# Optimization experiments

Hardware: AMD Instinct MI355X
Metric: run time of the kernel (lower is better)

## Reference

```python
import jax, jax.numpy as jnp
import numpy as np
from jax import lax

BN_EPS = 1e-5
ARC_EPS = 1e-7
M = 0.5   # margin
S = 64.0  # scale


def _conv_block(x, w, g, b, a, stride):
    # Conv2d(bias=False, VALID) + BatchNorm2d (training mode, batch stats) + PReLU
    y = lax.conv_general_dilated(x, w, (stride, stride), 'VALID',
                                 dimension_numbers=('NCHW', 'OIHW', 'NCHW'))
    mu = y.mean((0, 2, 3), keepdims=True)
    var = ((y - mu) ** 2).mean((0, 2, 3), keepdims=True)
    y = (y - mu) * lax.rsqrt(var + BN_EPS) * g.reshape(1, -1, 1, 1) + b.reshape(1, -1, 1, 1)
    return jnp.where(y > 0, y, a * y)


def setup_inputs() -> dict:
    key = jax.random.key(0)
    ks = jax.random.split(key, 16)
    N = 4096
    d = {}
    d['x'] = jax.random.normal(ks[0], (N, 1, 28, 28), jnp.float32)
    d['labels'] = jax.random.randint(ks[1], (N,), 0, 10)
    conv_shapes = [(32, 1, 1, 1), (64, 32, 3, 3), (32, 64, 1, 1),
                   (64, 32, 3, 3), (32, 64, 1, 1), (64, 32, 3, 3)]
    for i, s in enumerate(conv_shapes):
        fan_in = s[1] * s[2] * s[3]
        d[f'cw{i}'] = jax.random.normal(ks[2 + i], s, jnp.float32) / np.sqrt(fan_in)
        d[f'bg{i}'] = jnp.ones((s[0],), jnp.float32)
        d[f'bb{i}'] = jnp.zeros((s[0],), jnp.float32)
        d[f'pa{i}'] = jnp.full((), 0.25, jnp.float32)  # nn.PReLU() single param
    d['lw1'] = jax.random.normal(ks[8], (128, 1024), jnp.float32) * (1.0 / np.sqrt(1024))
    d['lg1'] = jnp.ones((128,), jnp.float32)
    d['lb1'] = jnp.zeros((128,), jnp.float32)
    d['pl1'] = jnp.full((), 0.25, jnp.float32)
    d['lw2'] = jax.random.normal(ks[9], (2, 128), jnp.float32) * (1.0 / np.sqrt(128))
    d['lb2'] = jnp.zeros((2,), jnp.float32)
    d['aw'] = jax.random.normal(ks[10], (10, 2), jnp.float32) * 0.2  # ArcLoss fc weight (out, in)
    return d


def reference(x, labels, cw0, cw1, cw2, cw3, cw4, cw5,
              bg0, bb0, bg1, bb1, bg2, bb2, bg3, bb3, bg4, bb4, bg5, bb5,
              pa0, pa1, pa2, pa3, pa4, pa5,
              lw1, lg1, lb1, pl1, lw2, lb2, aw):
    strides = (1, 2, 1, 2, 1, 1)
    ws = (cw0, cw1, cw2, cw3, cw4, cw5)
    gs = (bg0, bg1, bg2, bg3, bg4, bg5)
    bs = (bb0, bb1, bb2, bb3, bb4, bb5)
    pas = (pa0, pa1, pa2, pa3, pa4, pa5)
    h = x
    for w, g, b, a, st in zip(ws, gs, bs, pas, strides):
        h = _conv_block(h, w, g, b, a, st)  # final: (N, 64, 4, 4)
    flat = h.reshape(h.shape[0], -1)        # (N, 1024)
    z = flat @ lw1.T                         # (N, 128)
    mu = z.mean(0)
    var = ((z - mu) ** 2).mean(0)
    z = (z - mu) * lax.rsqrt(var + BN_EPS) * lg1 + lb1
    z = jnp.where(z > 0, z, pl1 * z)
    features = z @ lw2.T + lb2               # (N, 2)

    # ArcLoss. NOTE: original torch code's weight-normalization loop is a no-op
    # (rebinds local var), so fc weight is used UN-normalized; only x is normalized.
    xn = features / jnp.linalg.norm(features, axis=-1, keepdims=True)
    wf = xn @ aw.T                           # (N, 10) logits
    n = wf.shape[0]
    tgt = wf[jnp.arange(n), labels]          # vectorized diag gather
    num = S * jnp.cos(jnp.arccos(jnp.clip(tgt, -1.0 + ARC_EPS, 1.0 - ARC_EPS)) + M)
    # vectorized exclusion sum: sum_j exp(s*wf[i,j]) minus the target column
    den = jnp.exp(num) + jnp.sum(jnp.exp(S * wf), axis=1) - jnp.exp(S * tgt)
    loss = -jnp.mean(num - jnp.log(den))
    return (features, wf, loss)
```

## Files before the change

kernel.cpp:

```cpp
#include <hip/hip_runtime.h>
#include <hip/hip_bf16.h>
#include <hip/hip_fp16.h>
#include <math.h>


typedef __attribute__((ext_vector_type(8))) short s16x8;
typedef __attribute__((ext_vector_type(8))) _Float16 f16x8;
typedef __attribute__((ext_vector_type(2))) _Float16 h16x2;
typedef __attribute__((ext_vector_type(16))) float f32x16;

__device__ __forceinline__ unsigned short f2bf(float f) {
  __hip_bfloat16 h = __float2bfloat16(f);
  unsigned short u;
  __builtin_memcpy(&u, &h, 2);
  return u;
}
__device__ __forceinline__ float bf2f(unsigned short h) {
  union { unsigned int u; float f; } t; t.u = ((unsigned int)h) << 16; return t.f;
}
__device__ __forceinline__ unsigned short f2h(float f) {
  _Float16 h = (_Float16)f;
  unsigned short u;
  __builtin_memcpy(&u, &h, 2);
  return u;
}

__global__ __launch_bounds__(256) void kRedX(const float* __restrict__ x,
                                             float* __restrict__ part) {
  int tid = threadIdx.x;
  int b = blockIdx.x;
  const float4* x4 = (const float4*)x;
  float s = 0.f, q = 0.f;
  for (size_t i = (size_t)b * 256 + tid; i < 802816; i += (size_t)512 * 256) {
    float4 v = x4[i];
    s += v.x + v.y + v.z + v.w;
    q += v.x * v.x + v.y * v.y + v.z * v.z + v.w * v.w;
  }
#pragma unroll
  for (int off = 32; off; off >>= 1) {
    s += __shfl_down(s, off);
    q += __shfl_down(q, off);
  }
  __shared__ float ls[4][2];
  int w = tid >> 6;
  if ((tid & 63) == 0) { ls[w][0] = s; ls[w][1] = q; }
  __syncthreads();
  if (tid == 0) {
    part[b * 2]     = ls[0][0] + ls[1][0] + ls[2][0] + ls[3][0];
    part[b * 2 + 1] = ls[0][1] + ls[1][1] + ls[2][1] + ls[3][1];
  }
}

__global__ __launch_bounds__(256) void kRedPart(const float* __restrict__ part,
                                                float* __restrict__ outp, int nb, int C2) {
  int slot = blockIdx.x;
  int tid = threadIdx.x;
  float s = 0.f;
  for (int i = tid; i < nb; i += 256) s += part[(size_t)i * C2 + slot];
#pragma unroll
  for (int off = 32; off; off >>= 1) s += __shfl_down(s, off);
  __shared__ float ls[4];
  if ((tid & 63) == 0) ls[tid >> 6] = s;
  __syncthreads();
  if (tid == 0) outp[slot] = ls[0] + ls[1] + ls[2] + ls[3];
}

__global__ __launch_bounds__(256) void kPrepW(const float* __restrict__ cw1,
                                              unsigned short* __restrict__ wf) {
  int tid = threadIdx.x;
  int lane = tid & 63, fb = tid >> 6;
  int m = lane & 31, kg = lane >> 5;
  for (int pass = 0; pass < 9; pass++) {
    int f = pass * 4 + fb;
    int tap = f >> 2, rem = f & 3, kt = rem >> 1, nt = rem & 1;
    int o = nt * 32 + m;
    int kb = kt * 16 + kg * 8;
    union { s16x8 v; unsigned short e[8]; } u;
#pragma unroll
    for (int j = 0; j < 8; j++)
      u.e[j] = f2h(cw1[(size_t)o * 288 + (size_t)(kb + j) * 9 + tap]);
    ((s16x8*)wf)[f * 64 + lane] = u.v;
  }
}

__global__ __launch_bounds__(256) void kPrepW3(const float* __restrict__ cw3,
                                               unsigned short* __restrict__ wf3) {
  int tid = threadIdx.x;
  int lane = tid & 63, fq = tid >> 6;
  int m = lane & 31, kg = lane >> 5;
  for (int pass = 0; pass < 9; pass++) {
    int f = pass * 4 + fq;
    int s = f >> 1, nt = f & 1;
    int tap = s >> 1;
    int o = nt * 32 + m;
    int c0 = (s & 1) * 16 + kg * 8;
    union { s16x8 v; unsigned short e[8]; } u;
#pragma unroll
    for (int j = 0; j < 8; j++)
      u.e[j] = f2bf(cw3[(size_t)o * 288 + (size_t)(c0 + j) * 9 + tap]);
    ((s16x8*)wf3)[f * 64 + lane] = u.v;
  }
}

__global__ __launch_bounds__(256) void kPrepW1x1(const float* __restrict__ wgt,
                                                 unsigned short* __restrict__ wfb) {
  int tid = threadIdx.x;
  int l = tid & 63, ks = tid >> 6;
  int o = l & 31, kg = l >> 5;
  union { s16x8 v; unsigned short e[8]; } u;
#pragma unroll
  for (int j = 0; j < 8; j++) {
    int c = ks * 16 + kg * 8 + j;
    u.e[j] = f2bf(wgt[o * 64 + c]);
  }
  ((s16x8*)wfb)[ks * 64 + l] = u.v;
}

__global__ __launch_bounds__(256, 2) void kConv1(
    const float* __restrict__ x, const float* __restrict__ cw0,
    const float* __restrict__ bg0, const float* __restrict__ bb0,
    const float* __restrict__ pa0, const unsigned short* __restrict__ wf,
    const float* __restrict__ sx, unsigned short* __restrict__ y1b,
    float* __restrict__ part) {
  __shared__ __align__(16) unsigned short h0t[13440];
  __shared__ __align__(16) float xbuf[420];
  __shared__ float s0[32], t0[32];
  int tid = threadIdx.x;
  int n = blockIdx.x >> 1, half = blockIdx.x & 1;
  int l = tid & 63, w = tid >> 6;
  int nt = w & 1, mpair = w >> 1;
  int m = l & 31, kg = l >> 5;
  int npos = half ? 78 : 91;
  int xoff = half ? 392 : 0;
  int nxpix = half ? 364 : 420;

  f16x8 bfr[9][2];
  const f16x8* wfp = (const f16x8*)wf;
#pragma unroll
  for (int tap = 0; tap < 9; tap++)
#pragma unroll
    for (int kt = 0; kt < 2; kt++)
      bfr[tap][kt] = wfp[(tap * 4 + kt * 2 + nt) * 64 + l];

  {
    int nx4 = half ? 91 : 105;
    if (tid < nx4)
      ((float4*)xbuf)[tid] = ((const float4*)(x + (size_t)n * 784 + xoff))[tid];
  }
  if (tid < 32) {
    const float invM = 1.0f / (4096.0f * 784.0f);
    float mux = sx[0] * invM;
    float varx = fmaxf(sx[1] * invM - mux * mux, 0.0f);
    float w0 = cw0[tid];
    float inv = rsqrtf(w0 * w0 * varx + 1e-5f);
    float sc = w0 * bg0[tid] * inv;
    s0[tid] = sc;
    t0[tid] = bb0[tid] - mux * sc;
  }
  __syncthreads();

  float a0p = *pa0;
  _Float16 a1h = (_Float16)a0p;
  h16x2 a2 = {a1h, a1h};
  h16x2 z2 = {(_Float16)0.0f, (_Float16)0.0f};
  int g = tid & 3;
  h16x2 sg2[4], tg2[4];
#pragma unroll
  for (int j = 0; j < 4; j++) {
    sg2[j] = (h16x2){(_Float16)s0[g * 8 + 2 * j], (_Float16)s0[g * 8 + 2 * j + 1]};
    tg2[j] = (h16x2){(_Float16)t0[g * 8 + 2 * j], (_Float16)t0[g * 8 + 2 * j + 1]};
  }
  char* h0b = (char*)h0t;
  int koffW = g * 16;
  for (int t = 0; t < 7; t++) {
    int p = (tid >> 2) + t * 64;
    if (p < nxpix) {
      _Float16 xh = (_Float16)xbuf[p];
      h16x2 x2 = {xh, xh};
      union { f16x8 v; h16x2 h2[4]; } u;
#pragma unroll
      for (int j = 0; j < 4; j++) {
        h16x2 tv = x2 * sg2[j] + tg2[j];
        u.h2[j] = a2 * __builtin_elementwise_min(tv, z2) +
                  __builtin_elementwise_max(tv, z2);
      }
      int ad = ((p << 6) + koffW) ^ (((p >> 1) & 7) << 4);
      *(f16x8*)(h0b + ad) = u.v;
    }
  }
  __syncthreads();

  int tA = mpair ? 2 : 0;
  int lpA = tA * 32 + m; lpA = lpA > npos - 1 ? npos - 1 : lpA;
  int lpB = 32 + m;      lpB = lpB > npos - 1 ? npos - 1 : lpB;
  int pixbA = (lpA / 13) * 56 + (lpA % 13) * 2;
  int pixbB = (lpB / 13) * 56 + (lpB % 13) * 2;
  int koffA = kg * 16;

#define Z16 {0.f,0.f,0.f,0.f, 0.f,0.f,0.f,0.f, 0.f,0.f,0.f,0.f, 0.f,0.f,0.f,0.f}
  f32x16 acc0 = Z16, acc1 = Z16;

#define MT_STEP(ACC, PB) { \
  _Pragma("unroll") for (int tap = 0; tap < 9; tap++) { \
    int pix = (PB) + (tap / 3) * 28 + (tap % 3); \
    int ad = ((pix << 6) + koffA) ^ (((pix >> 1) & 7) << 4); \
    f16x8 a0 = *(const f16x8*)(h0b + ad); \
    f16x8 a1 = *(const f16x8*)(h0b + (ad ^ 32)); \
    ACC = __builtin_amdgcn_mfma_f32_32x32x16_f16(a0, bfr[tap][0], ACC, 0, 0, 0); \
    ACC = __builtin_amdgcn_mfma_f32_32x32x16_f16(a1, bfr[tap][1], ACC, 0, 0, 0); \
  } }

  MT_STEP(acc0, pixbA)
  if (mpair == 0) { MT_STEP(acc1, pixbB) }
#undef MT_STEP

  __syncthreads();
  unsigned short* ystage = h0t;
  float* sSf = xbuf;
  float* sQf = xbuf + 128;
  float s = 0.f, q = 0.f;
  int och = nt * 32 + m;
#define ST_MT(ACC, TILE) { int pbase = (TILE) * 32 + (kg << 2); \
  _Pragma("unroll") for (int r = 0; r < 16; r++) { \
    int p = pbase + (r & 3) + ((r >> 2) << 3); \
    if (p < npos) { float v = ACC[r]; \
      ystage[p * 64 + och] = f2bf(v); s += v; q += v * v; } } }

  ST_MT(acc0, tA)
  if (mpair == 0) { ST_MT(acc1, 1) }
#undef ST_MT

  s += __shfl_xor(s, 32);
  q += __shfl_xor(q, 32);
  if (l < 32) { sSf[w * 32 + l] = s; sQf[w * 32 + l] = q; }
  __syncthreads();
  {
    int nseg = npos * 8;
    const s16x8* src8 = (const s16x8*)ystage;
    s16x8* dst8 = (s16x8*)(y1b + (size_t)n * 10816 + half * 5824);
    for (int e = tid; e < nseg; e += 256) dst8[e] = src8[e];
  }
  if (tid < 64) {
    int o = tid, wv = o >> 5;
    part[(size_t)blockIdx.x * 128 + o] =
        sSf[wv * 32 + (o & 31)] + sSf[(wv + 2) * 32 + (o & 31)];
  } else if (tid < 128) {
    int o = tid - 64, wv = o >> 5;
    part[(size_t)blockIdx.x * 128 + 64 + o] =
        sQf[wv * 32 + (o & 31)] + sQf[(wv + 2) * 32 + (o & 31)];
  }
}

__global__ __launch_bounds__(256, 4) void kConv1x1m(
    const unsigned short* __restrict__ wfb, const float* __restrict__ g,
    const float* __restrict__ b, const float* __restrict__ pa,
    const float* __restrict__ stats, float invM,
    const unsigned short* __restrict__ in, unsigned short* __restrict__ outb,
    float* __restrict__ part) {
  __shared__ __align__(16) unsigned short hs[128 * 64];
  __shared__ float scs[64], shs[64];
  __shared__ float sS[4][32], sQ[4][32];
  int tid = threadIdx.x;
  size_t r0 = (size_t)blockIdx.x * 128;
  int l = tid & 63, w = tid >> 6;
  int m = l & 31, kg = l >> 5;

  s16x8 bfr[4];
  const s16x8* bp = (const s16x8*)wfb;
#pragma unroll
  for (int ks = 0; ks < 4; ks++) bfr[ks] = bp[ks * 64 + l];

  if (tid < 64) {
    float mu = stats[tid] * invM;
    float va = fmaxf(stats[64 + tid] * invM - mu * mu, 0.0f);
    float iv = rsqrtf(va + 1e-5f);
    float sc = g[tid] * iv;
    scs[tid] = sc;
    shs[tid] = b[tid] - mu * sc;
  }
  __syncthreads();
  float al = *pa;
  char* hb = (char*)hs;
#pragma unroll
  for (int i = 0; i < 4; i++) {
    int e = tid + i * 256;
    int row = e >> 3, seg = e & 7;
    union { s16x8 v; unsigned short e8[8]; } u, o8;
    u.v = *(const s16x8*)(in + (r0 + row) * 64 + seg * 8);
#pragma unroll
    for (int j = 0; j < 8; j++) {
      int c = seg * 8 + j;
      float h = fmaf(bf2f(u.e8[j]), scs[c], shs[c]);
      h = h > 0.f ? h : al * h;
      o8.e8[j] = f2bf(h);
    }
    int ad = (row * 128 + seg * 16) ^ ((row & 7) << 4);
    *(s16x8*)(hb + ad) = o8.v;
  }
  __syncthreads();

#define Z16 {0.f,0.f,0.f,0.f, 0.f,0.f,0.f,0.f, 0.f,0.f,0.f,0.f, 0.f,0.f,0.f,0.f}
  f32x16 acc = Z16;
#undef Z16
  int rloc = w * 32 + m;
  int abase = (rloc * 128 + kg * 16) ^ ((rloc & 7) << 4);
#pragma unroll
  for (int ks = 0; ks < 4; ks++) {
    s16x8 a = *(const s16x8*)(hb + (abase ^ (ks * 32)));
    acc = __builtin_amdgcn_mfma_f32_32x32x16_bf16(a, bfr[ks], acc, 0, 0, 0);
  }

  float ss = 0.f, qq = 0.f;
#pragma unroll
  for (int rr = 0; rr < 16; rr++) {
    int rowt = (rr & 3) + ((rr >> 2) << 3) + (kg << 2);
    float v = acc[rr];
    outb[(r0 + (size_t)w * 32 + rowt) * 32 + m] = f2bf(v);
    ss += v; qq += v * v;
  }
  ss += __shfl_xor(ss, 32);
  qq += __shfl_xor(qq, 32);
  if (l < 32) { sS[w][l] = ss; sQ[w][l] = qq; }
  __syncthreads();
  if (tid < 32) {
    part[(size_t)blockIdx.x * 64 + tid] = sS[0][tid] + sS[1][tid] + sS[2][tid] + sS[3][tid];
  } else if (tid < 64) {
    int o = tid - 32;
    part[(size_t)blockIdx.x * 64 + 32 + o] = sQ[0][o] + sQ[1][o] + sQ[2][o] + sQ[3][o];
  }
}

__global__ __launch_bounds__(256, 3) void kConv3m(
    const unsigned short* __restrict__ wf3, const float* __restrict__ g,
    const float* __restrict__ b, const float* __restrict__ pa,
    const float* __restrict__ stats, const unsigned short* __restrict__ in,
    unsigned short* __restrict__ outb, float* __restrict__ part) {
  __shared__ __align__(16) unsigned short h2t[169 * 32];
  __shared__ float scs[32], shs[32];
  __shared__ float sS[4][32], sQ[4][32];
  int tid = threadIdx.x;
  int n = blockIdx.x;
  int l = tid & 63, w = tid >> 6;
  int nt = w & 1, mt = w >> 1;
  int m = l & 31, kg = l >> 5;

  s16x8 bfr[18];
  const s16x8* wfp = (const s16x8*)wf3;
#pragma unroll
  for (int s = 0; s < 18; s++) bfr[s] = wfp[(s * 2 + nt) * 64 + l];

  if (tid < 32) {
    const float invM = 1.0f / 692224.0f;
    float mu = stats[tid] * invM;
    float va = fmaxf(stats[32 + tid] * invM - mu * mu, 0.0f);
    float iv = rsqrtf(va + 1e-5f);
    float sc = g[tid] * iv;
    scs[tid] = sc;
    shs[tid] = b[tid] - mu * sc;
  }
  __syncthreads();
  float al = *pa;
  char* hb = (char*)h2t;
  for (int e = tid; e < 676; e += 256) {
    int p = e >> 2, q = e & 3;
    union { s16x8 v; unsigned short e8[8]; } u, o8;
    u.v = ((const s16x8*)(in + ((size_t)n * 169 + p) * 32))[q];
#pragma unroll
    for (int j = 0; j < 8; j++) {
      int c = q * 8 + j;
      float h = fmaf(bf2f(u.e8[j]), scs[c], shs[c]);
      h = h > 0.f ? h : al * h;
      o8.e8[j] = f2bf(h);
    }
    int ad = ((p << 6) + q * 16) ^ (((p >> 1) & 7) << 4);
    *(s16x8*)(hb + ad) = o8.v;
  }
  __syncthreads();

  int p = mt * 32 + m;
  p = p > 35 ? 35 : p;
  int pixb = (p / 6) * 26 + (p % 6) * 2;

#define Z16 {0.f,0.f,0.f,0.f, 0.f,0.f,0.f,0.f, 0.f,0.f,0.f,0.f, 0.f,0.f,0.f,0.f}
  f32x16 acc = Z16;
#undef Z16
#pragma unroll
  for (int s = 0; s < 18; s++) {
    int tap = s >> 1;
    int pix = pixb + (tap / 3) * 13 + (tap % 3);
    int ad = ((pix << 6) + (s & 1) * 32 + kg * 16) ^ (((pix >> 1) & 7) << 4);
    s16x8 a = *(const s16x8*)(hb + ad);
    acc = __builtin_amdgcn_mfma_f32_32x32x16_bf16(a, bfr[s], acc, 0, 0, 0);
  }

  float ss = 0.f, qq = 0.f;
  int och = nt * 32 + m;
#pragma unroll
  for (int r = 0; r < 16; r++) {
    int row = (r & 3) + ((r >> 2) << 3) + (kg << 2);
    int pp = mt * 32 + row;
    if (pp < 36) {
      float v = acc[r];
      outb[((size_t)n * 36 + pp) * 64 + och] = f2bf(v);
      ss += v; qq += v * v;
    }
  }
  ss += __shfl_xor(ss, 32);
  qq += __shfl_xor(qq, 32);
  if (l < 32) { sS[w][l] = ss; sQ[w][l] = qq; }
  __syncthreads();
  if (tid < 64) {
    int o = tid, wv = o >> 5;
    part[(size_t)n * 128 + o] = sS[wv][o & 31] + sS[wv + 2][o & 31];
  } else if (tid < 128) {
    int o = tid - 64, wv = o >> 5;
    part[(size_t)n * 128 + 64 + o] = sQ[wv][o & 31] + sQ[wv + 2][o & 31];
  }
}

__global__ __launch_bounds__(128) void kConv5m(
    const unsigned short* __restrict__ wf5, const float* __restrict__ g,
    const float* __restrict__ b, const float* __restrict__ pa,
    const float* __restrict__ stats, const unsigned short* __restrict__ in,
    float* __restrict__ outb, float* __restrict__ part) {
  __shared__ __align__(16) unsigned short h4t[2 * 1280];
  __shared__ float scs[32], shs[32];
  int tid = threadIdx.x;
  int nA = blockIdx.x * 2;
  int l = tid & 63, w = tid >> 6;
  int m = l & 31, kg = l >> 5;

  s16x8 bfr[18];
  const s16x8* wfp = (const s16x8*)wf5;
#pragma unroll
  for (int s = 0; s < 18; s++) bfr[s] = wfp[(s * 2 + w) * 64 + l];

  if (tid < 32) {
    const float invM = 1.0f / 147456.0f;
    float mu = stats[tid] * invM;
    float va = fmaxf(stats[32 + tid] * invM - mu * mu, 0.0f);
    float iv = rsqrtf(va + 1e-5f);
    float sc = g[tid] * iv;
    scs[tid] = sc;
    shs[tid] = b[tid] - mu * sc;
  }
  __syncthreads();
  float al = *pa;
  char* hb = (char*)h4t;
  for (int e = tid; e < 288; e += 128) {
    int img = e >= 144;
    int rem = e - img * 144;
    int p = rem >> 2, q = rem & 3;
    union { s16x8 v; unsigned short e8[8]; } u, o8;
    u.v = ((const s16x8*)(in + ((size_t)(nA + img) * 36 + p) * 32))[q];
#pragma unroll
    for (int j = 0; j < 8; j++) {
      int c = q * 8 + j;
      float h = fmaf(bf2f(u.e8[j]), scs[c], shs[c]);
      h = h > 0.f ? h : al * h;
      o8.e8[j] = f2bf(h);
    }
    int ad = img * 2560 + (((p << 6) + q * 16) ^ (((p >> 1) & 7) << 4));
    *(s16x8*)(hb + ad) = o8.v;
  }
  __syncthreads();

  int imgl = m >> 4;
  int pl = m & 15;
  int pixb = (pl >> 2) * 6 + (pl & 3);
  int ibase = imgl * 2560;

#define Z16 {0.f,0.f,0.f,0.f, 0.f,0.f,0.f,0.f, 0.f,0.f,0.f,0.f, 0.f,0.f,0.f,0.f}
  f32x16 acc = Z16;
#undef Z16
#pragma unroll
  for (int s = 0; s < 18; s++) {
    int tap = s >> 1;
    int pix = pixb + (tap / 3) * 6 + (tap % 3);
    int ad = ibase + (((pix << 6) + (s & 1) * 32 + kg * 16) ^ (((pix >> 1) & 7) << 4));
    s16x8 a = *(const s16x8*)(hb + ad);
    acc = __builtin_amdgcn_mfma_f32_32x32x16_bf16(a, bfr[s], acc, 0, 0, 0);
  }

  float ss = 0.f, qq = 0.f;
  int och = w * 32 + m;
#pragma unroll
  for (int r = 0; r < 16; r++) {
    int row = (r & 3) + ((r >> 2) << 3) + (kg << 2);
    int img = row >> 4, p = row & 15;
    float v = acc[r];
    outb[(size_t)(nA + img) * 1024 + och * 16 + p] = v;
    ss += v; qq += v * v;
  }
  ss += __shfl_xor(ss, 32);
  qq += __shfl_xor(qq, 32);
  if (l < 32) {
    part[(size_t)blockIdx.x * 128 + w * 32 + l] = ss;
    part[(size_t)blockIdx.x * 128 + 64 + w * 32 + l] = qq;
  }
}

__global__ __launch_bounds__(256) void kPrepLW(const float* __restrict__ lw1,
                                               unsigned short* __restrict__ wfl) {
  int tid = threadIdx.x;
  int lane = tid & 63, fq = tid >> 6;
  int m = lane & 31, kg = lane >> 5;
  for (int pp = 0; pp < 4; pp++) {
    int f_idx = (blockIdx.x * 4 + pp) * 4 + fq;
    int ks = f_idx >> 2, nt = f_idx & 3;
    int f = nt * 32 + m;
    int kb = ks * 16 + kg * 8;
    const float4* src = (const float4*)(lw1 + (size_t)f * 1024 + kb);
    float4 v0 = src[0], v1 = src[1];
    float t[8] = {v0.x, v0.y, v0.z, v0.w, v1.x, v1.y, v1.z, v1.w};
    union { s16x8 v; unsigned short e[8]; } u;
#pragma unroll
    for (int j = 0; j < 8; j++) u.e[j] = f2bf(t[j]);
    ((s16x8*)wfl)[f_idx * 64 + lane] = u.v;
  }
}

__global__ __launch_bounds__(128) void kFC1m(
    const unsigned short* __restrict__ wfl, const float* __restrict__ g,
    const float* __restrict__ b, const float* __restrict__ pa,
    const float* __restrict__ stats, const float* __restrict__ y5,
    float* __restrict__ z, float* __restrict__ part) {
  __shared__ __align__(16) unsigned short hs[32 * 1024];
  __shared__ float scs[64], shs[64];
  int tid = threadIdx.x;
  int n0 = blockIdx.x * 32;
  if (tid < 64) {
    const float invM = 1.0f / 65536.0f;
    float mu = stats[tid] * invM;
    float va = fmaxf(stats[64 + tid] * invM - mu * mu, 0.0f);
    float iv = rsqrtf(va + 1e-5f);
    float sc = g[tid] * iv;
    scs[tid] = sc;
    shs[tid] = b[tid] - mu * sc;
  }
  __syncthreads();
  float al = *pa;
  char* hb = (char*)hs;
  for (int i = 0; i < 32; i++) {
    int sgi = tid + i * 128;
    int nn = sgi >> 7, k8 = sgi & 127;
    int c = k8 >> 1;
    float sc = scs[c], sh = shs[c];
    const float4* src = (const float4*)(y5 + (size_t)(n0 + nn) * 1024 + k8 * 8);
    float4 v0 = src[0], v1 = src[1];
    float t[8] = {v0.x, v0.y, v0.z, v0.w, v1.x, v1.y, v1.z, v1.w};
    union { s16x8 v; unsigned short e[8]; } u;
#pragma unroll
    for (int j = 0; j < 8; j++) {
      float h = fmaf(t[j], sc, sh);
      h = h > 0.f ? h : al * h;
      u.e[j] = f2bf(h);
    }
    int ad = (nn * 2048 + k8 * 16) ^ ((nn & 7) << 4);
    *(s16x8*)(hb + ad) = u.v;
  }
  __syncthreads();

  int l = tid & 63, w = tid >> 6;
  int m = l & 31, kg = l >> 5;
#define Z16 {0.f,0.f,0.f,0.f, 0.f,0.f,0.f,0.f, 0.f,0.f,0.f,0.f, 0.f,0.f,0.f,0.f}
  f32x16 acc0 = Z16, acc1 = Z16;
#undef Z16
  const s16x8* bp = (const s16x8*)wfl;
  int abase = (m * 2048 + kg * 16) ^ ((m & 7) << 4);
#pragma unroll 4
  for (int ks = 0; ks < 64; ks++) {
    s16x8 a = *(const s16x8*)(hb + (abase ^ (ks * 32)));
    s16x8 b0 = bp[(ks * 4 + 2 * w + 0) * 64 + l];
    s16x8 b1 = bp[(ks * 4 + 2 * w + 1) * 64 + l];
    acc0 = __builtin_amdgcn_mfma_f32_32x32x16_bf16(a, b0, acc0, 0, 0, 0);
    acc1 = __builtin_amdgcn_mfma_f32_32x32x16_bf16(a, b1, acc1, 0, 0, 0);
  }

  float s0 = 0.f, q0 = 0.f, s1 = 0.f, q1 = 0.f;
  int f0c = (2 * w) * 32 + m, f1c = (2 * w + 1) * 32 + m;
#pragma unroll
  for (int r = 0; r < 16; r++) {
    int n = (r & 3) + ((r >> 2) << 3) + (kg << 2);
    float v0 = acc0[r], v1 = acc1[r];
    z[(size_t)(n0 + n) * 128 + f0c] = v0;
    z[(size_t)(n0 + n) * 128 + f1c] = v1;
    s0 += v0; q0 += v0 * v0; s1 += v1; q1 += v1 * v1;
  }
  s0 += __shfl_xor(s0, 32); q0 += __shfl_xor(q0, 32);
  s1 += __shfl_xor(s1, 32); q1 += __shfl_xor(q1, 32);
  if (l < 32) {
    size_t base = (size_t)blockIdx.x * 256;
    part[base + w * 64 + m] = s0;
    part[base + w * 64 + 32 + m] = s1;
    part[base + 128 + w * 64 + m] = q0;
    part[base + 128 + w * 64 + 32 + m] = q1;
  }
}

__global__ __launch_bounds__(256) void kFC2Arc(
    const float* __restrict__ z, const float* __restrict__ s6,
    const float* __restrict__ lg1, const float* __restrict__ lb1,
    const float* __restrict__ pl1, const float* __restrict__ lw2,
    const float* __restrict__ lb2, const float* __restrict__ aw,
    const int* __restrict__ labels, float* __restrict__ out,
    float* __restrict__ lpart) {
  __shared__ float scz[128], shz[128], w2a[128], w2b[128];
  __shared__ float awl[20];
  __shared__ float lred[4];
  int tid = threadIdx.x;
  if (tid < 128) {
    const float invM = 1.0f / 4096.0f;
    float mu = s6[tid] * invM;
    float va = fmaxf(s6[128 + tid] * invM - mu * mu, 0.0f);
    float iv = rsqrtf(va + 1e-5f);
    float sc = lg1[tid] * iv;
    scz[tid] = sc;
    shz[tid] = lb1[tid] - mu * sc;
    w2a[tid] = lw2[tid];
    w2b[tid] = lw2[128 + tid];
  }
  if (tid < 20) awl[tid] = aw[tid];
  __syncthreads();
  float al = *pl1;
  int n = blockIdx.x * 256 + tid;
  const float4* zr = (const float4*)(z + (size_t)n * 128);
  float f0 = lb2[0], f1 = lb2[1];
#pragma unroll
  for (int kb = 0; kb < 32; kb++) {
    float4 v = zr[kb];
    float hv[4] = {v.x, v.y, v.z, v.w};
#pragma unroll
    for (int u = 0; u < 4; u++) {
      int k = kb * 4 + u;
      float h = fmaf(hv[u], scz[k], shz[k]);
      h = h > 0.f ? h : al * h;
      f0 = fmaf(h, w2a[k], f0);
      f1 = fmaf(h, w2b[k], f1);
    }
  }
  out[(size_t)n * 2] = f0;
  out[(size_t)n * 2 + 1] = f1;
  float nrm = sqrtf(fmaxf(f0 * f0 + f1 * f1, 1e-30f));
  float xn0 = f0 / nrm, xn1 = f1 / nrm;
  int lab = labels[n];
  float wv[10];
  float m64 = -3.4e38f;
#pragma unroll
  for (int j = 0; j < 10; j++) {
    float w = xn0 * awl[2 * j] + xn1 * awl[2 * j + 1];
    wv[j] = w;
    out[8192 + (size_t)n * 10 + j] = w;
    m64 = fmaxf(m64, 64.0f * w);
  }
  float tgt = wv[0];
#pragma unroll
  for (int j = 1; j < 10; j++) if (j == lab) tgt = wv[j];
  if (lab == 0) tgt = wv[0];
  const float CLO = (float)(-1.0 + 1e-7);
  const float CHI = (float)(1.0 - 1e-7);
  float t = fminf(fmaxf(tgt, CLO), CHI);
  float num = 64.0f * (t * 0.87758256189037276f - 0.47942553860420301f * sqrtf(fmaxf(1.0f - t * t, 0.0f)));
  float L = fmaxf(num, m64);
  float dsum = expf(num - L) - expf(64.0f * tgt - L);
#pragma unroll
  for (int j = 0; j < 10; j++) dsum += expf(64.0f * wv[j] - L);
  dsum = fmaxf(dsum, 1e-30f);
  float li = num - (L + logf(dsum));
#pragma unroll
  for (int off = 32; off; off >>= 1) li += __shfl_down(li, off);
  if ((tid & 63) == 0) lred[tid >> 6] = li;
  __syncthreads();
  if (tid == 0) lpart[blockIdx.x] = lred[0] + lred[1] + lred[2] + lred[3];
}

__global__ void kFinal(const float* __restrict__ lpart, float* __restrict__ out) {
  int tid = threadIdx.x;
  float v = (tid < 16) ? lpart[tid] : 0.f;
#pragma unroll
  for (int off = 8; off; off >>= 1) v += __shfl_down(v, off);
  if (tid == 0) out[49152] = -v * (1.0f / 4096.0f);
}

extern "C" void kernel_launch(void* const* d_in, const int* in_sizes, int n_in,
                              void* d_out, int out_size, void* d_ws, size_t ws_size,
                              hipStream_t stream) {
  const float* x   = (const float*)d_in[0];
  const int* labels = (const int*)d_in[1];
  const float* cw0 = (const float*)d_in[2];
  const float* bg0 = (const float*)d_in[3];
  const float* bb0 = (const float*)d_in[4];
  const float* pa0 = (const float*)d_in[5];
  const float* cw1 = (const float*)d_in[6];
  const float* bg1 = (const float*)d_in[7];
  const float* bb1 = (const float*)d_in[8];
  const float* pa1 = (const float*)d_in[9];
  const float* cw2 = (const float*)d_in[10];
  const float* bg2 = (const float*)d_in[11];
  const float* bb2 = (const float*)d_in[12];
  const float* pa2 = (const float*)d_in[13];
  const float* cw3 = (const float*)d_in[14];
  const float* bg3 = (const float*)d_in[15];
  const float* bb3 = (const float*)d_in[16];
  const float* pa3 = (const float*)d_in[17];
  const float* cw4 = (const float*)d_in[18];
  const float* bg4 = (const float*)d_in[19];
  const float* bb4 = (const float*)d_in[20];
  const float* pa4 = (const float*)d_in[21];
  const float* cw5 = (const float*)d_in[22];
  const float* bg5 = (const float*)d_in[23];
  const float* bb5 = (const float*)d_in[24];
  const float* pa5 = (const float*)d_in[25];
  const float* lw1 = (const float*)d_in[26];
  const float* lg1 = (const float*)d_in[27];
  const float* lb1 = (const float*)d_in[28];
  const float* pl1 = (const float*)d_in[29];
  const float* lw2 = (const float*)d_in[30];
  const float* lb2 = (const float*)d_in[31];
  const float* aw  = (const float*)d_in[32];
  float* out = (float*)d_out;
  float* ws = (float*)d_ws;

  float* PX = ws;
  float* SX = ws + 1024;
  float* S1 = ws + 1040;
  float* S2 = ws + 1168;
  float* S3 = ws + 1232;
  float* S4 = ws + 1360;
  float* S5 = ws + 1424;
  float* S6 = ws + 1552;
  float* LP = ws + 1808;
  float* P1 = ws + 2048;
  float* P2 = P1 + 1048576;
  float* P3 = P2 + 346112;
  float* P4 = P3 + 524288;
  float* P5 = P4 + 73728;
  float* P6 = P1;
  unsigned short* Y1 = (unsigned short*)(ws + (size_t)2359296);
  unsigned short* Y2 = Y1 + (size_t)44302336;
  unsigned short* Y3 = Y2 + (size_t)22151168;
  unsigned short* Y4 = Y3 + (size_t)9437184;
  float* Y5 = (float*)(Y4 + (size_t)4718592);
  float* Z  = Y5 + (size_t)4194304;
  float* WF = Z + 524288;
  float* WFL = WF + 16384;
  float* WF3 = WFL + 65536;
  float* WC2 = WF3 + 16384;
  float* WC4 = WC2 + 1024;
  float* WF5 = WC4 + 1024;

  kPrepW<<<1, 256, 0, stream>>>(cw1, (unsigned short*)WF);
  kPrepW3<<<1, 256, 0, stream>>>(cw3, (unsigned short*)WF3);
  kPrepW3<<<1, 256, 0, stream>>>(cw5, (unsigned short*)WF5);
  kPrepW1x1<<<1, 256, 0, stream>>>(cw2, (unsigned short*)WC2);
  kPrepW1x1<<<1, 256, 0, stream>>>(cw4, (unsigned short*)WC4);
  kPrepLW<<<16, 256, 0, stream>>>(lw1, (unsigned short*)WFL);
  kRedX<<<512, 256, 0, stream>>>(x, PX);
  kRedPart<<<2, 256, 0, stream>>>(PX, SX, 512, 2);
  kConv1<<<8192, 256, 0, stream>>>(x, cw0, bg0, bb0, pa0, (const unsigned short*)WF, SX, Y1, P1);
  kRedPart<<<128, 256, 0, stream>>>(P1, S1, 8192, 128);
  kConv1x1m<<<5408, 256, 0, stream>>>((const unsigned short*)WC2, bg1, bb1, pa1, S1,
                                      1.0f / 692224.0f, Y1, Y2, P2);
  kRedPart<<<64, 256, 0, stream>>>(P2, S2, 5408, 64);
  kConv3m<<<4096, 256, 0, stream>>>((const unsigned short*)WF3, bg2, bb2, pa2, S2, Y2, Y3, P3);
  kRedPart<<<128, 256, 0, stream>>>(P3, S3, 4096, 128);
  kConv1x1m<<<1152, 256, 0, stream>>>((const unsigned short*)WC4, bg3, bb3, pa3, S3,
                                      1.0f / 147456.0f, Y3, Y4, P4);
  kRedPart<<<64, 256, 0, stream>>>(P4, S4, 1152, 64);
  kConv5m<<<2048, 128, 0, stream>>>((const unsigned short*)WF5, bg4, bb4, pa4, S4, Y4, Y5, P5);
  kRedPart<<<128, 256, 0, stream>>>(P5, S5, 2048, 128);
  kFC1m<<<128, 128, 0, stream>>>((const unsigned short*)WFL, bg5, bb5, pa5, S5, Y5, Z, P6);
  kRedPart<<<256, 256, 0, stream>>>(P6, S6, 128, 256);
  kFC2Arc<<<16, 256, 0, stream>>>(Z, S6, lg1, lb1, pl1, lw2, lb2, aw, labels, out, LP);
  kFinal<<<1, 64, 0, stream>>>(LP, out);
}
```

Measured before the change: 235.8 us.

## Switch intermediate activations to fp16 with packed BN/PReLU and merge setup kernels

Intermediate activations and conv weights for the 1x1 and 3x3 blocks now use fp16 instead of bf16. The BN-affine plus PReLU prologue runs as packed half2 math, using min/max instead of per-element float conversions. The six weight-prep launches and the input reduction are merged into one kSetup kernel that dispatches on block index, cutting launch overhead. The cost is fp16 range and precision risk in the activations and the normalized values.

```diff
diff --git a/kernel.cpp b/kernel.cpp
--- a/kernel.cpp
+++ b/kernel.cpp
@@ -25,10 +25,8 @@
   return u;
 }
 
-__global__ __launch_bounds__(256) void kRedX(const float* __restrict__ x,
-                                             float* __restrict__ part) {
-  int tid = threadIdx.x;
-  int b = blockIdx.x;
+__device__ void dRedX(const float* __restrict__ x, float* __restrict__ part, int b) {
+  int tid = threadIdx.x;
   const float4* x4 = (const float4*)x;
   float s = 0.f, q = 0.f;
   for (size_t i = (size_t)b * 256 + tid; i < 802816; i += (size_t)512 * 256) {
@@ -51,22 +49,7 @@
   }
 }
 
-__global__ __launch_bounds__(256) void kRedPart(const float* __restrict__ part,
-                                                float* __restrict__ outp, int nb, int C2) {
-  int slot = blockIdx.x;
-  int tid = threadIdx.x;
-  float s = 0.f;
-  for (int i = tid; i < nb; i += 256) s += part[(size_t)i * C2 + slot];
-#pragma unroll
-  for (int off = 32; off; off >>= 1) s += __shfl_down(s, off);
-  __shared__ float ls[4];
-  if ((tid & 63) == 0) ls[tid >> 6] = s;
-  __syncthreads();
-  if (tid == 0) outp[slot] = ls[0] + ls[1] + ls[2] + ls[3];
-}
-
-__global__ __launch_bounds__(256) void kPrepW(const float* __restrict__ cw1,
-                                              unsigned short* __restrict__ wf) {
+__device__ void dPrepW(const float* __restrict__ cw1, unsigned short* __restrict__ wf) {
   int tid = threadIdx.x;
   int lane = tid & 63, fb = tid >> 6;
   int m = lane & 31, kg = lane >> 5;
@@ -83,8 +66,7 @@
   }
 }
 
-__global__ __launch_bounds__(256) void kPrepW3(const float* __restrict__ cw3,
-                                               unsigned short* __restrict__ wf3) {
+__device__ void dPrepW3(const float* __restrict__ cw, unsigned short* __restrict__ wf3) {
   int tid = threadIdx.x;
   int lane = tid & 63, fq = tid >> 6;
   int m = lane & 31, kg = lane >> 5;
@@ -97,13 +79,12 @@
     union { s16x8 v; unsigned short e[8]; } u;
 #pragma unroll
     for (int j = 0; j < 8; j++)
-      u.e[j] = f2bf(cw3[(size_t)o * 288 + (size_t)(c0 + j) * 9 + tap]);
+      u.e[j] = f2h(cw[(size_t)o * 288 + (size_t)(c0 + j) * 9 + tap]);
     ((s16x8*)wf3)[f * 64 + lane] = u.v;
   }
 }
 
-__global__ __launch_bounds__(256) void kPrepW1x1(const float* __restrict__ wgt,
-                                                 unsigned short* __restrict__ wfb) {
+__device__ void dPrepW1x1(const float* __restrict__ wgt, unsigned short* __restrict__ wfb) {
   int tid = threadIdx.x;
   int l = tid & 63, ks = tid >> 6;
   int o = l & 31, kg = l >> 5;
@@ -111,9 +92,60 @@
 #pragma unroll
   for (int j = 0; j < 8; j++) {
     int c = ks * 16 + kg * 8 + j;
-    u.e[j] = f2bf(wgt[o * 64 + c]);
+    u.e[j] = f2h(wgt[o * 64 + c]);
   }
   ((s16x8*)wfb)[ks * 64 + l] = u.v;
+}
+
+__device__ void dPrepLW(const float* __restrict__ lw1, unsigned short* __restrict__ wfl, int blk) {
+  int tid = threadIdx.x;
+  int lane = tid & 63, fq = tid >> 6;
+  int m = lane & 31, kg = lane >> 5;
+  for (int pp = 0; pp < 4; pp++) {
+    int f_idx = (blk * 4 + pp) * 4 + fq;
+    int ks = f_idx >> 2, nt = f_idx & 3;
+    int f = nt * 32 + m;
+    int kb = ks * 16 + kg * 8;
+    const float4* src = (const float4*)(lw1 + (size_t)f * 1024 + kb);
+    float4 v0 = src[0], v1 = src[1];
+    float t[8] = {v0.x, v0.y, v0.z, v0.w, v1.x, v1.y, v1.z, v1.w};
+    union { s16x8 v; unsigned short e[8]; } u;
+#pragma unroll
+    for (int j = 0; j < 8; j++) u.e[j] = f2bf(t[j]);
+    ((s16x8*)wfl)[f_idx * 64 + lane] = u.v;
+  }
+}
+
+__global__ __launch_bounds__(256) void kSetup(
+    const float* __restrict__ x, float* __restrict__ PX,
+    const float* __restrict__ cw1, unsigned short* __restrict__ WF,
+    const float* __restrict__ cw3, unsigned short* __restrict__ WF3,
+    const float* __restrict__ cw5, unsigned short* __restrict__ WF5,
+    const float* __restrict__ cw2, unsigned short* __restrict__ WC2,
+    const float* __restrict__ cw4, unsigned short* __restrict__ WC4,
+    const float* __restrict__ lw1, unsigned short* __restrict__ WFL) {
+  int b = blockIdx.x;
+  if (b < 512)       dRedX(x, PX, b);
+  else if (b == 512) dPrepW(cw1, WF);
+  else if (b == 513) dPrepW3(cw3, WF3);
+  else if (b == 514) dPrepW3(cw5, WF5);
+  else if (b == 515) dPrepW1x1(cw2, WC2);
+  else if (b == 516) dPrepW1x1(cw4, WC4);
+  else               dPrepLW(lw1, WFL, b - 517);
+}
+
+__global__ __launch_bounds__(256) void kRedPart(const float* __restrict__ part,
+                                                float* __restrict__ outp, int nb, int C2) {
+  int slot = blockIdx.x;
+  int tid = threadIdx.x;
+  float s = 0.f;
+  for (int i = tid; i < nb; i += 256) s += part[(size_t)i * C2 + slot];
+#pragma unroll
+  for (int off = 32; off; off >>= 1) s += __shfl_down(s, off);
+  __shared__ float ls[4];
+  if ((tid & 63) == 0) ls[tid >> 6] = s;
+  __syncthreads();
+  if (tid == 0) outp[slot] = ls[0] + ls[1] + ls[2] + ls[3];
 }
 
 __global__ __launch_bounds__(256, 2) void kConv1(
@@ -224,7 +256,7 @@
   _Pragma("unroll") for (int r = 0; r < 16; r++) { \
     int p = pbase + (r & 3) + ((r >> 2) << 3); \
     if (p < npos) { float v = ACC[r]; \
-      ystage[p * 64 + och] = f2bf(v); s += v; q += v * v; } } }
+      ystage[p * 64 + och] = f2h(v); s += v; q += v * v; } } }
 
   ST_MT(acc0, tA)
   if (mpair == 0) { ST_MT(acc1, 1) }
@@ -265,8 +297,8 @@
   int l = tid & 63, w = tid >> 6;
   int m = l & 31, kg = l >> 5;
 
-  s16x8 bfr[4];
-  const s16x8* bp = (const s16x8*)wfb;
+  f16x8 bfr[4];
+  const f16x8* bp = (const f16x8*)wfb;
 #pragma unroll
   for (int ks = 0; ks < 4; ks++) bfr[ks] = bp[ks * 64 + l];
 
@@ -280,22 +312,32 @@
   }
   __syncthreads();
   float al = *pa;
+  _Float16 alh = (_Float16)al;
+  h16x2 a2 = {alh, alh};
+  h16x2 z2 = {(_Float16)0.0f, (_Float16)0.0f};
+  int seg0 = tid & 7;
+  h16x2 sc2[4], sh2[4];
+#pragma unroll
+  for (int j = 0; j < 4; j++) {
+    int c = seg0 * 8 + 2 * j;
+    sc2[j] = (h16x2){(_Float16)scs[c], (_Float16)scs[c + 1]};
+    sh2[j] = (h16x2){(_Float16)shs[c], (_Float16)shs[c + 1]};
+  }
   char* hb = (char*)hs;
 #pragma unroll
   for (int i = 0; i < 4; i++) {
     int e = tid + i * 256;
-    int row = e >> 3, seg = e & 7;
-    union { s16x8 v; unsigned short e8[8]; } u, o8;
-    u.v = *(const s16x8*)(in + (r0 + row) * 64 + seg * 8);
-#pragma unroll
-    for (int j = 0; j < 8; j++) {
-      int c = seg * 8 + j;
-      float h = fmaf(bf2f(u.e8[j]), scs[c], shs[c]);
-      h = h > 0.f ? h : al * h;
-      o8.e8[j] = f2bf(h);
+    int row = e >> 3;
+    union { f16x8 v; h16x2 h2[4]; } u, o8;
+    u.v = *(const f16x8*)(in + (r0 + row) * 64 + seg0 * 8);
+#pragma unroll
+    for (int j = 0; j < 4; j++) {
+      h16x2 tv = u.h2[j] * sc2[j] + sh2[j];
+      o8.h2[j] = a2 * __builtin_elementwise_min(tv, z2) +
+                 __builtin_elementwise_max(tv, z2);
     }
-    int ad = (row * 128 + seg * 16) ^ ((row & 7) << 4);
-    *(s16x8*)(hb + ad) = o8.v;
+    int ad = (row * 128 + seg0 * 16) ^ ((row & 7) << 4);
+    *(f16x8*)(hb + ad) = o8.v;
   }
   __syncthreads();
 
@@ -306,8 +348,8 @@
   int abase = (rloc * 128 + kg * 16) ^ ((rloc & 7) << 4);
 #pragma unroll
   for (int ks = 0; ks < 4; ks++) {
-    s16x8 a = *(const s16x8*)(hb + (abase ^ (ks * 32)));
-    acc = __builtin_amdgcn_mfma_f32_32x32x16_bf16(a, bfr[ks], acc, 0, 0, 0);
+    f16x8 a = *(const f16x8*)(hb + (abase ^ (ks * 32)));
+    acc = __builtin_amdgcn_mfma_f32_32x32x16_f16(a, bfr[ks], acc, 0, 0, 0);
   }
 
   float ss = 0.f, qq = 0.f;
@@ -315,7 +357,7 @@
   for (int rr = 0; rr < 16; rr++) {
     int rowt = (rr & 3) + ((rr >> 2) << 3) + (kg << 2);
     float v = acc[rr];
-    outb[(r0 + (size_t)w * 32 + rowt) * 32 + m] = f2bf(v);
+    outb[(r0 + (size_t)w * 32 + rowt) * 32 + m] = f2h(v);
     ss += v; qq += v * v;
   }
   ss += __shfl_xor(ss, 32);
@@ -344,8 +386,8 @@
   int nt = w & 1, mt = w >> 1;
   int m = l & 31, kg = l >> 5;
 
-  s16x8 bfr[18];
-  const s16x8* wfp = (const s16x8*)wf3;
+  f16x8 bfr[18];
+  const f16x8* wfp = (const f16x8*)wf3;
 #pragma unroll
   for (int s = 0; s < 18; s++) bfr[s] = wfp[(s * 2 + nt) * 64 + l];
 
@@ -360,20 +402,30 @@
   }
   __syncthreads();
   float al = *pa;
+  _Float16 alh = (_Float16)al;
+  h16x2 a2 = {alh, alh};
+  h16x2 z2 = {(_Float16)0.0f, (_Float16)0.0f};
+  int q0 = tid & 3;
+  h16x2 sc2[4], sh2[4];
+#pragma unroll
+  for (int j = 0; j < 4; j++) {
+    int c = q0 * 8 + 2 * j;
+    sc2[j] = (h16x2){(_Float16)scs[c], (_Float16)scs[c + 1]};
+    sh2[j] = (h16x2){(_Float16)shs[c], (_Float16)shs[c + 1]};
+  }
   char* hb = (char*)h2t;
   for (int e = tid; e < 676; e += 256) {
-    int p = e >> 2, q = e & 3;
-    union { s16x8 v; unsigned short e8[8]; } u, o8;
-    u.v = ((const s16x8*)(in + ((size_t)n * 169 + p) * 32))[q];
-#pragma unroll
-    for (int j = 0; j < 8; j++) {
-      int c = q * 8 + j;
-      float h = fmaf(bf2f(u.e8[j]), scs[c], shs[c]);
-      h = h > 0.f ? h : al * h;
-      o8.e8[j] = f2bf(h);
+    int p = e >> 2;
+    union { f16x8 v; h16x2 h2[4]; } u, o8;
+    u.v = ((const f16x8*)(in + ((size_t)n * 169 + p) * 32))[q0];
+#pragma unroll
+    for (int j = 0; j < 4; j++) {
+      h16x2 tv = u.h2[j] * sc2[j] + sh2[j];
+      o8.h2[j] = a2 * __builtin_elementwise_min(tv, z2) +
+                 __builtin_elementwise_max(tv, z2);
     }
-    int ad = ((p << 6) + q * 16) ^ (((p >> 1) & 7) << 4);
-    *(s16x8*)(hb + ad) = o8.v;
+    int ad = ((p << 6) + q0 * 16) ^ (((p >> 1) & 7) << 4);
+    *(f16x8*)(hb + ad) = o8.v;
   }
   __syncthreads();
 
@@ -389,8 +441,8 @@
     int tap = s >> 1;
     int pix = pixb + (tap / 3) * 13 + (tap % 3);
     int ad = ((pix << 6) + (s & 1) * 32 + kg * 16) ^ (((pix >> 1) & 7) << 4);
-    s16x8 a = *(const s16x8*)(hb + ad);
-    acc = __builtin_amdgcn_mfma_f32_32x32x16_bf16(a, bfr[s], acc, 0, 0, 0);
+    f16x8 a = *(const f16x8*)(hb + ad);
+    acc = __builtin_amdgcn_mfma_f32_32x32x16_f16(a, bfr[s], acc, 0, 0, 0);
   }
 
   float ss = 0.f, qq = 0.f;
@@ -401,7 +453,7 @@
     int pp = mt * 32 + row;
     if (pp < 36) {
       float v = acc[r];
-      outb[((size_t)n * 36 + pp) * 64 + och] = f2bf(v);
+      outb[((size_t)n * 36 + pp) * 64 + och] = f2h(v);
       ss += v; qq += v * v;
     }
   }
@@ -430,8 +482,8 @@
   int l = tid & 63, w = tid >> 6;
   int m = l & 31, kg = l >> 5;
 
-  s16x8 bfr[18];
-  const s16x8* wfp = (const s16x8*)wf5;
+  f16x8 bfr[18];
+  const f16x8* wfp = (const f16x8*)wf5;
 #pragma unroll
   for (int s = 0; s < 18; s++) bfr[s] = wfp[(s * 2 + w) * 64 + l];
 
@@ -446,22 +498,32 @@
   }
   __syncthreads();
   float al = *pa;
+  _Float16 alh = (_Float16)al;
+  h16x2 a2 = {alh, alh};
+  h16x2 z2 = {(_Float16)0.0f, (_Float16)0.0f};
+  int q0 = tid & 3;
+  h16x2 sc2[4], sh2[4];
+#pragma unroll
+  for (int j = 0; j < 4; j++) {
+    int c = q0 * 8 + 2 * j;
+    sc2[j] = (h16x2){(_Float16)scs[c], (_Float16)scs[c + 1]};
+    sh2[j] = (h16x2){(_Float16)shs[c], (_Float16)shs[c + 1]};
+  }
   char* hb = (char*)h4t;
   for (int e = tid; e < 288; e += 128) {
     int img = e >= 144;
     int rem = e - img * 144;
-    int p = rem >> 2, q = rem & 3;
-    union { s16x8 v; unsigned short e8[8]; } u, o8;
-    u.v = ((const s16x8*)(in + ((size_t)(nA + img) * 36 + p) * 32))[q];
-#pragma unroll
-    for (int j = 0; j < 8; j++) {
-      int c = q * 8 + j;
-      float h = fmaf(bf2f(u.e8[j]), scs[c], shs[c]);
-      h = h > 0.f ? h : al * h;
-      o8.e8[j] = f2bf(h);
+    int p = rem >> 2;
+    union { f16x8 v; h16x2 h2[4]; } u, o8;
+    u.v = ((const f16x8*)(in + ((size_t)(nA + img) * 36 + p) * 32))[q0];
+#pragma unroll
+    for (int j = 0; j < 4; j++) {
+      h16x2 tv = u.h2[j] * sc2[j] + sh2[j];
+      o8.h2[j] = a2 * __builtin_elementwise_min(tv, z2) +
+                 __builtin_elementwise_max(tv, z2);
     }
-    int ad = img * 2560 + (((p << 6) + q * 16) ^ (((p >> 1) & 7) << 4));
-    *(s16x8*)(hb + ad) = o8.v;
+    int ad = img * 2560 + (((p << 6) + q0 * 16) ^ (((p >> 1) & 7) << 4));
+    *(f16x8*)(hb + ad) = o8.v;
   }
   __syncthreads();
 
@@ -478,8 +540,8 @@
     int tap = s >> 1;
     int pix = pixb + (tap / 3) * 6 + (tap % 3);
     int ad = ibase + (((pix << 6) + (s & 1) * 32 + kg * 16) ^ (((pix >> 1) & 7) << 4));
-    s16x8 a = *(const s16x8*)(hb + ad);
-    acc = __builtin_amdgcn_mfma_f32_32x32x16_bf16(a, bfr[s], acc, 0, 0, 0);
+    f16x8 a = *(const f16x8*)(hb + ad);
+    acc = __builtin_amdgcn_mfma_f32_32x32x16_f16(a, bfr[s], acc, 0, 0, 0);
   }
 
   float ss = 0.f, qq = 0.f;
@@ -497,26 +559,6 @@
   if (l < 32) {
     part[(size_t)blockIdx.x * 128 + w * 32 + l] = ss;
     part[(size_t)blockIdx.x * 128 + 64 + w * 32 + l] = qq;
-  }
-}
-
-__global__ __launch_bounds__(256) void kPrepLW(const float* __restrict__ lw1,
-                                               unsigned short* __restrict__ wfl) {
-  int tid = threadIdx.x;
-  int lane = tid & 63, fq = tid >> 6;
-  int m = lane & 31, kg = lane >> 5;
-  for (int pp = 0; pp < 4; pp++) {
-    int f_idx = (blockIdx.x * 4 + pp) * 4 + fq;
-    int ks = f_idx >> 2, nt = f_idx & 3;
-    int f = nt * 32 + m;
-    int kb = ks * 16 + kg * 8;
-    const float4* src = (const float4*)(lw1 + (size_t)f * 1024 + kb);
-    float4 v0 = src[0], v1 = src[1];
-    float t[8] = {v0.x, v0.y, v0.z, v0.w, v1.x, v1.y, v1.z, v1.w};
-    union { s16x8 v; unsigned short e[8]; } u;
-#pragma unroll
-    for (int j = 0; j < 8; j++) u.e[j] = f2bf(t[j]);
-    ((s16x8*)wfl)[f_idx * 64 + lane] = u.v;
   }
 }
 
@@ -749,13 +791,12 @@
   float* WC4 = WC2 + 1024;
   float* WF5 = WC4 + 1024;
 
-  kPrepW<<<1, 256, 0, stream>>>(cw1, (unsigned short*)WF);
-  kPrepW3<<<1, 256, 0, stream>>>(cw3, (unsigned short*)WF3);
-  kPrepW3<<<1, 256, 0, stream>>>(cw5, (unsigned short*)WF5);
-  kPrepW1x1<<<1, 256, 0, stream>>>(cw2, (unsigned short*)WC2);
-  kPrepW1x1<<<1, 256, 0, stream>>>(cw4, (unsigned short*)WC4);
-  kPrepLW<<<16, 256, 0, stream>>>(lw1, (unsigned short*)WFL);
-  kRedX<<<512, 256, 0, stream>>>(x, PX);
+  kSetup<<<533, 256, 0, stream>>>(x, PX, cw1, (unsigned short*)WF,
+                                  cw3, (unsigned short*)WF3,
+                                  cw5, (unsigned short*)WF5,
+                                  cw2, (unsigned short*)WC2,
+                                  cw4, (unsigned short*)WC4,
+                                  lw1, (unsigned short*)WFL);
   kRedPart<<<2, 256, 0, stream>>>(PX, SX, 512, 2);
   kConv1<<<8192, 256, 0, stream>>>(x, cw0, bg0, bb0, pa0, (const unsigned short*)WF, SX, Y1, P1);
   kRedPart<<<128, 256, 0, stream>>>(P1, S1, 8192, 128);
```

After: 209.1 us (median of 2 runs). 11.3% less time.
